# Kernel tuning notes

Hardware: AMD Instinct MI355X
Metric: run time of the kernel (lower is better)

## Reference

```python
import jax, jax.numpy as jnp
import numpy as np

B, N, C, E = 4, 20000, 64, 320000

def setup_inputs() -> dict:
    key = jax.random.key(0)
    ks = jax.random.split(key, 9)
    s = 0.1
    return {
        "x": jax.random.normal(ks[0], (B, N, C), jnp.float32),
        "edge_index": jax.random.randint(ks[1], (2, E), 0, N, jnp.int64),
        "lin_w": jax.random.normal(ks[2], (C, C), jnp.float32) * s,
        "bias": jnp.zeros((C,), jnp.float32),
        "up1_w": jax.random.normal(ks[3], (C, C), jnp.float32) * s,
        "up2_w": jax.random.normal(ks[4], (C, C), jnp.float32) * s,
        "lo1_w": jax.random.normal(ks[5], (C, C), jnp.float32) * s,
        "lo2_w": jax.random.normal(ks[6], (C, C), jnp.float32) * s,
        "last_w": jax.random.normal(ks[7], (2 * C, 2 * C), jnp.float32) * s,
    }

def reference(x, edge_index, lin_w, bias, up1_w, up2_w, lo1_w, lo2_w, last_w):
    n = x.shape[1]
    # add self loops (PyG add_self_loops)
    loops = jnp.arange(n, dtype=edge_index.dtype)
    row = jnp.concatenate([edge_index[0], loops])  # source
    col = jnp.concatenate([edge_index[1], loops])  # target
    # linear transform (Linear with no bias: x @ W^T)
    h = jnp.einsum("bnc,oc->bno", x, lin_w)
    # symmetric degree normalization; degree computed on col (targets)
    deg = jax.ops.segment_sum(jnp.ones_like(col, dtype=h.dtype), col, num_segments=n)
    dis = jnp.where(deg > 0, deg ** -0.5, 0.0)
    norm = dis[row] * dis[col]  # [E+N]
    # gather / scale / scatter-add (GCN propagate with aggr='add')
    msg = h[:, row, :] * norm[None, :, None]          # [B, E+N, C]
    agg = jax.ops.segment_sum(jnp.swapaxes(msg, 0, 1), col, num_segments=n)  # [N, B, C]
    out = jnp.swapaxes(agg, 0, 1) + bias              # [B, N, C]
    fst = jax.nn.sigmoid(out)
    upper = jnp.einsum("bnc,oc->bno", jnp.einsum("bnc,oc->bno", fst, up1_w), up2_w)
    lower = jnp.einsum("bnc,oc->bno", jnp.einsum("bnc,oc->bno", fst, lo1_w), lo2_w)
    combined = jnp.concatenate([upper, lower], axis=2)  # [B, N, 2C]
    last = jnp.einsum("bnc,oc->bno", combined, last_w)
    return jax.nn.relu(last)
```

## Files before the change

kernel.cpp:

```cpp
#include <hip/hip_runtime.h>
#include <cstdint>
#include <cstddef>

#define NODES 20000
#define NEDGE 320000
#define CAP 64
#define SCATB 625
#define LINB 16
#define BIGB 32
#define XCVB 5000
#define BLDB (SCATB + LINB + BIGB + XCVB)

using bf16x8 = __attribute__((ext_vector_type(8))) __bf16;
using f32x4  = __attribute__((ext_vector_type(4))) float;
using f32x2  = __attribute__((ext_vector_type(2))) float;
using us8    = __attribute__((ext_vector_type(8))) unsigned short;

__device__ __forceinline__ unsigned short f2bf(float f) {
  union { float f; unsigned int u; } v; v.f = f;
  unsigned int r = v.u + 0x7FFF + ((v.u >> 16) & 1);
  return (unsigned short)(r >> 16);
}

#define DECFMA(u, dr, s0, s1, s2, s3)                           \
  {                                                             \
    f32x2 lo_ = __builtin_amdgcn_cvt_pk_f32_fp8(u, false);      \
    f32x2 hi_ = __builtin_amdgcn_cvt_pk_f32_fp8(u, true);       \
    s0 += dr * lo_.x; s1 += dr * lo_.y;                         \
    s2 += dr * hi_.x; s3 += dr * hi_.y;                         \
  }

__global__ void k_build(const int* __restrict__ ei, int* __restrict__ cnt,
                        unsigned short* __restrict__ csr16,
                        const float* __restrict__ lin, const float* __restrict__ u1,
                        const float* __restrict__ u2, const float* __restrict__ l1,
                        const float* __restrict__ l2, const float* __restrict__ lastw,
                        unsigned short* __restrict__ wb16,
                        const float* __restrict__ x, unsigned int* __restrict__ xs8) {
  __shared__ float tmp_u[4][64];
  __shared__ float tmp_l[4][64];
  int bid = blockIdx.x, t = threadIdx.x;
  if (bid < SCATB) {
    int i = (bid * 256 + t) * 2;
    int2 r2 = *(const int2*)(ei + i);
    int2 c2 = *(const int2*)(ei + NEDGE + i);
    int p0 = atomicAdd(&cnt[c2.x], 1);
    if (p0 < CAP) csr16[c2.x * CAP + p0] = (unsigned short)r2.x;
    int p1 = atomicAdd(&cnt[c2.y], 1);
    if (p1 < CAP) csr16[c2.y * CAP + p1] = (unsigned short)r2.y;
  } else if (bid < SCATB + LINB) {
    int g = (bid - SCATB) * 256 + t;
    wb16[g] = f2bf(lin[g]);
  } else if (bid < SCATB + LINB + BIGB) {
    int o0 = (bid - SCATB - LINB) * 4;
    int ol = t >> 6, p = t & 63;
    float su = 0.f, sl = 0.f;
    for (int k = 0; k < 64; ++k) {
      float lu = lastw[(o0 + ol) * 128 + k];
      float ll = lastw[(o0 + ol) * 128 + 64 + k];
      su += lu * u2[k * 64 + p];
      sl += ll * l2[k * 64 + p];
    }
    tmp_u[ol][p] = su;
    tmp_l[ol][p] = sl;
    __syncthreads();
    float acc = 0.f;
    for (int q = 0; q < 64; ++q)
      acc += tmp_u[ol][q] * u1[q * 64 + p] + tmp_l[ol][q] * l1[q * 64 + p];
    wb16[4096 + (o0 + ol) * 64 + p] = f2bf(acc);
  } else {
    int g = (bid - SCATB - LINB - BIGB) * 256 + t;
    int n = g >> 6, i = g & 63;
    int b = i >> 4, c = (i & 15) * 4;
    f32x4 v = __builtin_nontemporal_load(
        (const f32x4*)(x + ((size_t)b * NODES + n) * 64 + c));
    int p = 0;
    p = __builtin_amdgcn_cvt_pk_fp8_f32(v.x, v.y, p, false);
    p = __builtin_amdgcn_cvt_pk_fp8_f32(v.z, v.w, p, true);
    xs8[(size_t)n * 64 + i] = (unsigned int)p;
  }
}

__global__ __launch_bounds__(512) void k_gpost(const int* __restrict__ cnt,
                                               const unsigned short* __restrict__ csr16,
                                               const unsigned int* __restrict__ xs8,
                                               const float* __restrict__ bias,
                                               const unsigned short* __restrict__ wb16,
                                               float* __restrict__ out) {
  __shared__ unsigned short xa[32][72];
  __shared__ unsigned short fst[32][72];
  int t = threadIdx.x;
  int w = t >> 6, l = t & 63;
  int n0 = blockIdx.x * 8;
  int n = n0 + w;

  int cn = cnt[n];
  int dn = cn > CAP ? CAP : cn;
  float dsn = rsqrtf((float)(cn + 1));
  int base = n * CAP;

  us8 rr0 = *(const us8*)(csr16 + base);
  us8 rr1 = *(const us8*)(csr16 + base + 8);
  us8 rr2 = *(const us8*)(csr16 + base + 16);
  unsigned int uself = xs8[(size_t)n * 64 + l];

  float a0, a1, a2, a3;
  {
    f32x2 lo = __builtin_amdgcn_cvt_pk_f32_fp8(uself, false);
    f32x2 hi = __builtin_amdgcn_cvt_pk_f32_fp8(uself, true);
    a0 = dsn * lo.x; a1 = dsn * lo.y; a2 = dsn * hi.x; a3 = dsn * hi.y;
  }

  {
    int r[16]; int c[16]; unsigned int uu[16];
#pragma unroll
    for (int j = 0; j < 16; ++j) {
      int rj = (j < 8) ? (int)rr0[j] : (int)rr1[j - 8];
      r[j] = (j < dn) ? rj : n;
    }
#pragma unroll
    for (int j = 0; j < 16; ++j) c[j] = cnt[r[j]];
#pragma unroll
    for (int j = 0; j < 16; ++j) uu[j] = xs8[(size_t)r[j] * 64 + l];
#pragma unroll
    for (int j = 0; j < 16; ++j) {
      float dj = (j < dn) ? rsqrtf((float)(c[j] + 1)) : 0.f;
      DECFMA(uu[j], dj, a0, a1, a2, a3);
    }
  }
  if (dn > 16) {
    {
      int r[8]; int c[8]; unsigned int uu[8];
#pragma unroll
      for (int j = 0; j < 8; ++j) {
        int rj = (int)rr2[j];
        r[j] = (16 + j < dn) ? rj : n;
      }
#pragma unroll
      for (int j = 0; j < 8; ++j) c[j] = cnt[r[j]];
#pragma unroll
      for (int j = 0; j < 8; ++j) uu[j] = xs8[(size_t)r[j] * 64 + l];
#pragma unroll
      for (int j = 0; j < 8; ++j) {
        float dj = (16 + j < dn) ? rsqrtf((float)(c[j] + 1)) : 0.f;
        DECFMA(uu[j], dj, a0, a1, a2, a3);
      }
    }
    for (int i = 24; i < dn; i += 8) {
      us8 rv = *(const us8*)(csr16 + base + i);
      int r[8]; int c[8]; unsigned int uu[8];
#pragma unroll
      for (int j = 0; j < 8; ++j) {
        int rj = (int)rv[j];
        r[j] = (i + j < dn) ? rj : n;
      }
#pragma unroll
      for (int j = 0; j < 8; ++j) c[j] = cnt[r[j]];
#pragma unroll
      for (int j = 0; j < 8; ++j) uu[j] = xs8[(size_t)r[j] * 64 + l];
#pragma unroll
      for (int j = 0; j < 8; ++j) {
        float dj = (i + j < dn) ? rsqrtf((float)(c[j] + 1)) : 0.f;
        DECFMA(uu[j], dj, a0, a1, a2, a3);
      }
    }
  }

  {
    ushort4 o;
    o.x = f2bf(a0); o.y = f2bf(a1); o.z = f2bf(a2); o.w = f2bf(a3);
    *(ushort4*)&xa[w * 4 + (l >> 4)][(l & 15) * 4] = o;
  }

  int m = l & 15, q = l >> 4;
  const unsigned short* wlin = wb16;
  const unsigned short* bigw = wb16 + 4096;
  int ws1 = w & 3;

  bf16x8 wa0 = *(const bf16x8*)(wlin + (16 * ws1 + m) * 64 + q * 8);
  bf16x8 wa1 = *(const bf16x8*)(wlin + (16 * ws1 + m) * 64 + q * 8 + 32);
  bf16x8 wbk0 = *(const bf16x8*)(bigw + (16 * w + m) * 64 + q * 8);
  bf16x8 wbk1 = *(const bf16x8*)(bigw + (16 * w + m) * 64 + q * 8 + 32);
  float4 b4 = *(const float4*)(bias + 16 * ws1 + 4 * q);
  float ds0 = rsqrtf((float)(cnt[n0 + (m >> 2)] + 1));
  float ds1 = rsqrtf((float)(cnt[n0 + 4 + (m >> 2)] + 1));

  __syncthreads();

  if (w < 4) {
    f32x4 acc10 = {0, 0, 0, 0}, acc11 = {0, 0, 0, 0};
    bf16x8 x00 = *(const bf16x8*)&xa[m][q * 8];
    bf16x8 x10 = *(const bf16x8*)&xa[16 + m][q * 8];
    acc10 = __builtin_amdgcn_mfma_f32_16x16x32_bf16(wa0, x00, acc10, 0, 0, 0);
    acc11 = __builtin_amdgcn_mfma_f32_16x16x32_bf16(wa0, x10, acc11, 0, 0, 0);
    bf16x8 x01 = *(const bf16x8*)&xa[m][q * 8 + 32];
    bf16x8 x11 = *(const bf16x8*)&xa[16 + m][q * 8 + 32];
    acc10 = __builtin_amdgcn_mfma_f32_16x16x32_bf16(wa1, x01, acc10, 0, 0, 0);
    acc11 = __builtin_amdgcn_mfma_f32_16x16x32_bf16(wa1, x11, acc11, 0, 0, 0);
    {
      float v0 = acc10[0] * ds0 + b4.x;
      float v1 = acc10[1] * ds0 + b4.y;
      float v2 = acc10[2] * ds0 + b4.z;
      float v3 = acc10[3] * ds0 + b4.w;
      ushort4 o;
      o.x = f2bf(1.f / (1.f + __expf(-v0)));
      o.y = f2bf(1.f / (1.f + __expf(-v1)));
      o.z = f2bf(1.f / (1.f + __expf(-v2)));
      o.w = f2bf(1.f / (1.f + __expf(-v3)));
      *(ushort4*)&fst[m][16 * ws1 + 4 * q] = o;
    }
    {
      float v0 = acc11[0] * ds1 + b4.x;
      float v1 = acc11[1] * ds1 + b4.y;
      float v2 = acc11[2] * ds1 + b4.z;
      float v3 = acc11[3] * ds1 + b4.w;
      ushort4 o;
      o.x = f2bf(1.f / (1.f + __expf(-v0)));
      o.y = f2bf(1.f / (1.f + __expf(-v1)));
      o.z = f2bf(1.f / (1.f + __expf(-v2)));
      o.w = f2bf(1.f / (1.f + __expf(-v3)));
      *(ushort4*)&fst[16 + m][16 * ws1 + 4 * q] = o;
    }
  }
  __syncthreads();

  {
    f32x4 a00 = {0, 0, 0, 0}, a01 = {0, 0, 0, 0};
    bf16x8 f00 = *(const bf16x8*)&fst[m][q * 8];
    bf16x8 f10 = *(const bf16x8*)&fst[16 + m][q * 8];
    a00 = __builtin_amdgcn_mfma_f32_16x16x32_bf16(f00, wbk0, a00, 0, 0, 0);
    a01 = __builtin_amdgcn_mfma_f32_16x16x32_bf16(f10, wbk0, a01, 0, 0, 0);
    bf16x8 f01 = *(const bf16x8*)&fst[m][q * 8 + 32];
    bf16x8 f11 = *(const bf16x8*)&fst[16 + m][q * 8 + 32];
    a00 = __builtin_amdgcn_mfma_f32_16x16x32_bf16(f01, wbk1, a00, 0, 0, 0);
    a01 = __builtin_amdgcn_mfma_f32_16x16x32_bf16(f11, wbk1, a01, 0, 0, 0);

#pragma unroll
    for (int nt = 0; nt < 2; ++nt) {
      f32x4 acc = nt == 0 ? a00 : a01;
#pragma unroll
      for (int r = 0; r < 4; ++r) {
        int row = 16 * nt + 4 * q + r;
        int nn = n0 + (row >> 2), b = row & 3;
        float v = acc[r];
        __builtin_nontemporal_store(
            v > 0.f ? v : 0.f,
            out + ((size_t)b * NODES + nn) * 128 + 16 * w + m);
      }
    }
  }
}

extern "C" void kernel_launch(void* const* d_in, const int* in_sizes, int n_in,
                              void* d_out, int out_size, void* d_ws, size_t ws_size,
                              hipStream_t stream) {
  const float* x     = (const float*)d_in[0];
  const int*   ei    = (const int*)d_in[1];
  const float* lin_w = (const float*)d_in[2];
  const float* bias  = (const float*)d_in[3];
  const float* up1   = (const float*)d_in[4];
  const float* up2   = (const float*)d_in[5];
  const float* lo1   = (const float*)d_in[6];
  const float* lo2   = (const float*)d_in[7];
  const float* lastw = (const float*)d_in[8];
  float* out = (float*)d_out;

  char* ws = (char*)d_ws;
  unsigned short* wb16  = (unsigned short*)(ws);
  int*            cnt   = (int*)(ws + (192 << 10));
  unsigned short* csr16 = (unsigned short*)(ws + (1 << 20));
  unsigned int*   xs8   = (unsigned int*)(ws + (8 << 20));

  (void)hipMemsetAsync(cnt, 0, NODES * sizeof(int), stream);
  k_build<<<BLDB, 256, 0, stream>>>(ei, cnt, csr16, lin_w, up1, up2, lo1, lo2,
                                    lastw, wb16, x, xs8);
  k_gpost<<<NODES / 8, 512, 0, stream>>>(cnt, csr16, xs8, bias, wb16, out);
}
```

Baseline: 135.2 us.

## Shrink gather-post block to 4 nodes and 256 threads, remap MFMA work per wave

Halves the fused gather+MLP block from 8 nodes/512 threads to 4 nodes/256 threads. All four waves now run the first linear MFMA instead of only half of them idling, and each wave computes two 16-column output tiles of the final matmul. This removes idle waves in the first GEMM stage and shortens per-block barrier waits, at the cost of twice as many blocks, more per-wave weight register loads, and reloading weights per smaller block.

```diff
diff --git a/kernel.cpp b/kernel.cpp
--- a/kernel.cpp
+++ b/kernel.cpp
@@ -81,17 +81,17 @@
   }
 }
 
-__global__ __launch_bounds__(512) void k_gpost(const int* __restrict__ cnt,
+__global__ __launch_bounds__(256) void k_gpost(const int* __restrict__ cnt,
                                                const unsigned short* __restrict__ csr16,
                                                const unsigned int* __restrict__ xs8,
                                                const float* __restrict__ bias,
                                                const unsigned short* __restrict__ wb16,
                                                float* __restrict__ out) {
-  __shared__ unsigned short xa[32][72];
-  __shared__ unsigned short fst[32][72];
+  __shared__ unsigned short xa[16][72];
+  __shared__ unsigned short fst[16][72];
   int t = threadIdx.x;
   int w = t >> 6, l = t & 63;
-  int n0 = blockIdx.x * 8;
+  int n0 = blockIdx.x * 4;
   int n = n0 + w;
 
   int cn = cnt[n];
@@ -175,77 +175,57 @@
   int m = l & 15, q = l >> 4;
   const unsigned short* wlin = wb16;
   const unsigned short* bigw = wb16 + 4096;
-  int ws1 = w & 3;
-
-  bf16x8 wa0 = *(const bf16x8*)(wlin + (16 * ws1 + m) * 64 + q * 8);
-  bf16x8 wa1 = *(const bf16x8*)(wlin + (16 * ws1 + m) * 64 + q * 8 + 32);
-  bf16x8 wbk0 = *(const bf16x8*)(bigw + (16 * w + m) * 64 + q * 8);
-  bf16x8 wbk1 = *(const bf16x8*)(bigw + (16 * w + m) * 64 + q * 8 + 32);
-  float4 b4 = *(const float4*)(bias + 16 * ws1 + 4 * q);
+
+  bf16x8 wa0  = *(const bf16x8*)(wlin + (16 * w + m) * 64 + q * 8);
+  bf16x8 wa1  = *(const bf16x8*)(wlin + (16 * w + m) * 64 + q * 8 + 32);
+  bf16x8 wb00 = *(const bf16x8*)(bigw + (32 * w + m) * 64 + q * 8);
+  bf16x8 wb10 = *(const bf16x8*)(bigw + (32 * w + 16 + m) * 64 + q * 8);
+  bf16x8 wb01 = *(const bf16x8*)(bigw + (32 * w + m) * 64 + q * 8 + 32);
+  bf16x8 wb11 = *(const bf16x8*)(bigw + (32 * w + 16 + m) * 64 + q * 8 + 32);
+  float4 b4 = *(const float4*)(bias + 16 * w + 4 * q);
   float ds0 = rsqrtf((float)(cnt[n0 + (m >> 2)] + 1));
-  float ds1 = rsqrtf((float)(cnt[n0 + 4 + (m >> 2)] + 1));
 
   __syncthreads();
 
-  if (w < 4) {
-    f32x4 acc10 = {0, 0, 0, 0}, acc11 = {0, 0, 0, 0};
+  {
+    f32x4 acc1 = {0, 0, 0, 0};
     bf16x8 x00 = *(const bf16x8*)&xa[m][q * 8];
-    bf16x8 x10 = *(const bf16x8*)&xa[16 + m][q * 8];
-    acc10 = __builtin_amdgcn_mfma_f32_16x16x32_bf16(wa0, x00, acc10, 0, 0, 0);
-    acc11 = __builtin_amdgcn_mfma_f32_16x16x32_bf16(wa0, x10, acc11, 0, 0, 0);
+    acc1 = __builtin_amdgcn_mfma_f32_16x16x32_bf16(wa0, x00, acc1, 0, 0, 0);
     bf16x8 x01 = *(const bf16x8*)&xa[m][q * 8 + 32];
-    bf16x8 x11 = *(const bf16x8*)&xa[16 + m][q * 8 + 32];
-    acc10 = __builtin_amdgcn_mfma_f32_16x16x32_bf16(wa1, x01, acc10, 0, 0, 0);
-    acc11 = __builtin_amdgcn_mfma_f32_16x16x32_bf16(wa1, x11, acc11, 0, 0, 0);
-    {
-      float v0 = acc10[0] * ds0 + b4.x;
-      float v1 = acc10[1] * ds0 + b4.y;
-      float v2 = acc10[2] * ds0 + b4.z;
-      float v3 = acc10[3] * ds0 + b4.w;
-      ushort4 o;
-      o.x = f2bf(1.f / (1.f + __expf(-v0)));
-      o.y = f2bf(1.f / (1.f + __expf(-v1)));
-      o.z = f2bf(1.f / (1.f + __expf(-v2)));
-      o.w = f2bf(1.f / (1.f + __expf(-v3)));
-      *(ushort4*)&fst[m][16 * ws1 + 4 * q] = o;
-    }
-    {
-      float v0 = acc11[0] * ds1 + b4.x;
-      float v1 = acc11[1] * ds1 + b4.y;
-      float v2 = acc11[2] * ds1 + b4.z;
-      float v3 = acc11[3] * ds1 + b4.w;
-      ushort4 o;
-      o.x = f2bf(1.f / (1.f + __expf(-v0)));
-      o.y = f2bf(1.f / (1.f + __expf(-v1)));
-      o.z = f2bf(1.f / (1.f + __expf(-v2)));
-      o.w = f2bf(1.f / (1.f + __expf(-v3)));
-      *(ushort4*)&fst[16 + m][16 * ws1 + 4 * q] = o;
-    }
+    acc1 = __builtin_amdgcn_mfma_f32_16x16x32_bf16(wa1, x01, acc1, 0, 0, 0);
+    float v0 = acc1[0] * ds0 + b4.x;
+    float v1 = acc1[1] * ds0 + b4.y;
+    float v2 = acc1[2] * ds0 + b4.z;
+    float v3 = acc1[3] * ds0 + b4.w;
+    ushort4 o;
+    o.x = f2bf(1.f / (1.f + __expf(-v0)));
+    o.y = f2bf(1.f / (1.f + __expf(-v1)));
+    o.z = f2bf(1.f / (1.f + __expf(-v2)));
+    o.w = f2bf(1.f / (1.f + __expf(-v3)));
+    *(ushort4*)&fst[m][16 * w + 4 * q] = o;
   }
   __syncthreads();
 
   {
-    f32x4 a00 = {0, 0, 0, 0}, a01 = {0, 0, 0, 0};
+    f32x4 am0 = {0, 0, 0, 0}, am1 = {0, 0, 0, 0};
     bf16x8 f00 = *(const bf16x8*)&fst[m][q * 8];
-    bf16x8 f10 = *(const bf16x8*)&fst[16 + m][q * 8];
-    a00 = __builtin_amdgcn_mfma_f32_16x16x32_bf16(f00, wbk0, a00, 0, 0, 0);
-    a01 = __builtin_amdgcn_mfma_f32_16x16x32_bf16(f10, wbk0, a01, 0, 0, 0);
+    am0 = __builtin_amdgcn_mfma_f32_16x16x32_bf16(f00, wb00, am0, 0, 0, 0);
+    am1 = __builtin_amdgcn_mfma_f32_16x16x32_bf16(f00, wb10, am1, 0, 0, 0);
     bf16x8 f01 = *(const bf16x8*)&fst[m][q * 8 + 32];
-    bf16x8 f11 = *(const bf16x8*)&fst[16 + m][q * 8 + 32];
-    a00 = __builtin_amdgcn_mfma_f32_16x16x32_bf16(f01, wbk1, a00, 0, 0, 0);
-    a01 = __builtin_amdgcn_mfma_f32_16x16x32_bf16(f11, wbk1, a01, 0, 0, 0);
-
-#pragma unroll
-    for (int nt = 0; nt < 2; ++nt) {
-      f32x4 acc = nt == 0 ? a00 : a01;
+    am0 = __builtin_amdgcn_mfma_f32_16x16x32_bf16(f01, wb01, am0, 0, 0, 0);
+    am1 = __builtin_amdgcn_mfma_f32_16x16x32_bf16(f01, wb11, am1, 0, 0, 0);
+
+#pragma unroll
+    for (int mt = 0; mt < 2; ++mt) {
+      f32x4 acc = mt == 0 ? am0 : am1;
 #pragma unroll
       for (int r = 0; r < 4; ++r) {
-        int row = 16 * nt + 4 * q + r;
+        int row = 4 * q + r;
         int nn = n0 + (row >> 2), b = row & 3;
         float v = acc[r];
         __builtin_nontemporal_store(
             v > 0.f ? v : 0.f,
-            out + ((size_t)b * NODES + nn) * 128 + 16 * w + m);
+            out + ((size_t)b * NODES + nn) * 128 + 32 * w + 16 * mt + m);
       }
     }
   }
@@ -274,5 +254,5 @@
   (void)hipMemsetAsync(cnt, 0, NODES * sizeof(int), stream);
   k_build<<<BLDB, 256, 0, stream>>>(ei, cnt, csr16, lin_w, up1, up2, lo1, lo2,
                                     lastw, wb16, x, xs8);
-  k_gpost<<<NODES / 8, 512, 0, stream>>>(cnt, csr16, xs8, bias, wb16, out);
-}
+  k_gpost<<<NODES / 4, 256, 0, stream>>>(cnt, csr16, xs8, bias, wb16, out);
+}
```

Measured after the change: 139.1 us. +3.0%, slower.
